# Optimization experiments

Hardware: AMD Instinct MI355X
Metric: run time of the kernel (lower is better)

The kernel has to match this reference:

```python
import jax, jax.numpy as jnp
import numpy as np

B, S, D, H = 2, 2048, 1024, 16
DK = D // H


def setup_inputs() -> dict:
    key = jax.random.key(0)
    ks = jax.random.split(key, 10)
    scale = 1.0 / np.sqrt(D)
    x = jax.random.normal(ks[0], (B, S, D), dtype=jnp.float32)
    # causal mask: 1 = attend, 0 = masked (module's create_causal_mask)
    mask = jnp.tril(jnp.ones((S, S), dtype=jnp.int32))[None, None]
    Wq = jax.random.normal(ks[1], (D, D), jnp.float32) * scale
    bq = jax.random.normal(ks[2], (D,), jnp.float32) * 0.01
    Wk = jax.random.normal(ks[3], (D, D), jnp.float32) * scale
    bk = jax.random.normal(ks[4], (D,), jnp.float32) * 0.01
    Wv = jax.random.normal(ks[5], (D, D), jnp.float32) * scale
    bv = jax.random.normal(ks[6], (D,), jnp.float32) * 0.01
    Wo = jax.random.normal(ks[7], (D, D), jnp.float32) * scale
    bo = jax.random.normal(ks[8], (D,), jnp.float32) * 0.01
    return {"x": x, "mask": mask, "Wq": Wq, "bq": bq, "Wk": Wk, "bk": bk,
            "Wv": Wv, "bv": bv, "Wo": Wo, "bo": bo}


def reference(x, mask, Wq, bq, Wk, bk, Wv, bv, Wo, bo):
    b, s, _ = x.shape
    # projections; [B,S,D] -> [B,H,S,DK]
    def split_heads(t):
        return t.reshape(b, s, H, DK).transpose(0, 2, 1, 3)
    Q = split_heads(x @ Wq + bq)
    K = split_heads(x @ Wk + bk)
    V = split_heads(x @ Wv + bv)
    scores = jnp.einsum('bhqd,bhkd->bhqk', Q, K) / np.sqrt(DK)
    scores = jnp.where(mask == 0, jnp.float32(-1e9), scores)
    attn = jax.nn.softmax(scores, axis=-1)  # dropout p=0 -> identity
    ctx = jnp.einsum('bhqk,bhkd->bhqd', attn, V)
    ctx = ctx.transpose(0, 2, 1, 3).reshape(b, s, D)
    return ctx @ Wo + bo
```

## Files before the change

kernel.cpp:

```cpp
#include <hip/hip_runtime.h>
#include <hip/hip_bf16.h>


typedef _Float16 f16x8 __attribute__((ext_vector_type(8)));
typedef _Float16 f16x4 __attribute__((ext_vector_type(4)));
typedef _Float16 f16x2 __attribute__((ext_vector_type(2)));
typedef float f32x4 __attribute__((ext_vector_type(4)));

#define QSCALE 0.180336880111112f

__device__ __forceinline__ void async_copy16(const _Float16* gsrc,
                                             _Float16* ldst) {
  __builtin_amdgcn_global_load_lds(
      (const __attribute__((address_space(1))) void*)gsrc,
      (__attribute__((address_space(3))) void*)ldst, 16, 0, 0);
}

__global__ __launch_bounds__(256) void prep(
    const float* __restrict__ x, _Float16* __restrict__ xh,
    const float* __restrict__ W0, const float* __restrict__ W1,
    const float* __restrict__ W2, const float* __restrict__ W3,
    _Float16* __restrict__ T0, _Float16* __restrict__ T1,
    _Float16* __restrict__ T2, _Float16* __restrict__ T3) {
  if (blockIdx.x < 4096) {
    int i = (blockIdx.x * 256 + threadIdx.x) * 4;
    float4 v = *(const float4*)(x + i);
    f16x4 o;
    o.x = (_Float16)v.x; o.y = (_Float16)v.y;
    o.z = (_Float16)v.z; o.w = (_Float16)v.w;
    *(f16x4*)(xh + i) = o;
    return;
  }
  const int id = blockIdx.x - 4096;
  const int w = id >> 10, rem = id & 1023;
  const int bx = rem & 31, by = rem >> 5;
  const float* W; _Float16* T;
  switch (w) {
    case 0: W = W0; T = T0; break;
    case 1: W = W1; T = T1; break;
    case 2: W = W2; T = T2; break;
    default: W = W3; T = T3; break;
  }
  __shared__ _Float16 tile[32][33];
  const int tx = threadIdx.x & 31, ty = threadIdx.x >> 5;
  const int n0 = bx * 32, k0 = by * 32;
  for (int i = 0; i < 4; i++) {
    int kk = k0 + ty + i * 8;
    tile[ty + i * 8][tx] = (_Float16)W[(size_t)kk * 1024 + n0 + tx];
  }
  __syncthreads();
  for (int i = 0; i < 4; i++) {
    int nn = n0 + ty + i * 8;
    T[(size_t)nn * 1024 + k0 + tx] = tile[tx][ty + i * 8];
  }
}

__global__ __launch_bounds__(256) void gemm_qkv(
    const _Float16* __restrict__ A, const _Float16* __restrict__ BtAll,
    const float* __restrict__ bq, const float* __restrict__ bk,
    const float* __restrict__ bv, _Float16* __restrict__ Qh,
    _Float16* __restrict__ Kh, _Float16* __restrict__ VT) {
  __shared__ _Float16 As[128 * 32];
  __shared__ _Float16 Bs[128 * 32];
  const int tid = threadIdx.x;
  const int wave = tid >> 6, lane = tid & 63;
  const int lr = lane & 15, lq = lane >> 4;
  const int m0 = blockIdx.x * 128, n0 = blockIdx.y * 128;
  const int rw = (wave & 1) * 64, cw = (wave >> 1) * 64;

  const int sel = blockIdx.y >> 3;
  const float* bias = sel == 0 ? bq : (sel == 1 ? bk : bv);
  const int c0 = n0 & 1023;

  f32x4 acc[4][4] = {};
  const int r0 = wave * 32 + (lane >> 2);
  const int woff = (lane & 3) * 8;

  for (int kt = 0; kt < 1024; kt += 32) {
    __syncthreads();
    async_copy16(A + (size_t)(m0 + r0) * 1024 + kt + woff, As + r0 * 32 + woff);
    async_copy16(A + (size_t)(m0 + r0 + 16) * 1024 + kt + woff,
                 As + (r0 + 16) * 32 + woff);
    async_copy16(BtAll + (size_t)(n0 + r0) * 1024 + kt + woff,
                 Bs + r0 * 32 + woff);
    async_copy16(BtAll + (size_t)(n0 + r0 + 16) * 1024 + kt + woff,
                 Bs + (r0 + 16) * 32 + woff);
    __syncthreads();
    f16x8 af[4], bf[4];
    for (int i = 0; i < 4; i++)
      af[i] = *(const f16x8*)(As + (rw + i * 16 + lr) * 32 + lq * 8);
    for (int j = 0; j < 4; j++)
      bf[j] = *(const f16x8*)(Bs + (cw + j * 16 + lr) * 32 + lq * 8);
    for (int i = 0; i < 4; i++)
      for (int j = 0; j < 4; j++)
        acc[i][j] = __builtin_amdgcn_mfma_f32_16x16x32_f16(af[i], bf[j],
                                                           acc[i][j], 0, 0, 0);
  }

  if (sel == 2) {
    for (int i = 0; i < 4; i++) {
      const int row = m0 + rw + i * 16 + lq * 4;
      const int bb = row >> 11, ss = row & 2047;
      for (int j = 0; j < 4; j++) {
        const int col = c0 + cw + j * 16 + lr;
        const int hh = col >> 6, dk = col & 63;
        const float bvl = bias[col];
        f16x4 pv;
        for (int r = 0; r < 4; r++) pv[r] = (_Float16)(acc[i][j][r] + bvl);
        *(f16x4*)(VT + ((size_t)(bb * 16 + hh) * 64 + dk) * 2048 + ss) = pv;
      }
    }
  } else {
    _Float16* out = sel == 0 ? Qh : Kh;
    const float scl = sel == 0 ? QSCALE : 1.0f;
    for (int i = 0; i < 4; i++) {
      const int row = m0 + rw + i * 16 + lq * 4;
      for (int j = 0; j < 4; j++) {
        const int col = c0 + cw + j * 16 + lr;
        const float bvl = bias[col];
        for (int r = 0; r < 4; r++)
          out[(size_t)(row + r) * 1024 + col] =
              (_Float16)((acc[i][j][r] + bvl) * scl);
      }
    }
  }
}

__global__ __launch_bounds__(256) void gemm_out(
    const _Float16* __restrict__ A, const _Float16* __restrict__ Bt,
    const float* __restrict__ bias, float* __restrict__ out) {
  __shared__ _Float16 As[128 * 32];
  __shared__ _Float16 Bs[64 * 32];
  const int tid = threadIdx.x;
  const int wave = tid >> 6, lane = tid & 63;
  const int lr = lane & 15, lq = lane >> 4;
  const int m0 = blockIdx.x * 128, n0 = blockIdx.y * 64;
  const int rw = (wave & 1) * 64, cw = (wave >> 1) * 32;
  f32x4 acc[4][2] = {};
  const int r0 = wave * 32 + (lane >> 2);
  const int br = tid >> 2;
  const int woff = (lane & 3) * 8;

  for (int kt = 0; kt < 1024; kt += 32) {
    __syncthreads();
    async_copy16(A + (size_t)(m0 + r0) * 1024 + kt + woff, As + r0 * 32 + woff);
    async_copy16(A + (size_t)(m0 + r0 + 16) * 1024 + kt + woff,
                 As + (r0 + 16) * 32 + woff);
    async_copy16(Bt + (size_t)(n0 + br) * 1024 + kt + woff,
                 Bs + br * 32 + woff);
    __syncthreads();
    f16x8 af[4], bf[2];
    for (int i = 0; i < 4; i++)
      af[i] = *(const f16x8*)(As + (rw + i * 16 + lr) * 32 + lq * 8);
    for (int j = 0; j < 2; j++)
      bf[j] = *(const f16x8*)(Bs + (cw + j * 16 + lr) * 32 + lq * 8);
    for (int i = 0; i < 4; i++)
      for (int j = 0; j < 2; j++)
        acc[i][j] = __builtin_amdgcn_mfma_f32_16x16x32_f16(af[i], bf[j],
                                                           acc[i][j], 0, 0, 0);
  }
  for (int i = 0; i < 4; i++) {
    const int row = m0 + rw + i * 16 + lq * 4;
    for (int j = 0; j < 2; j++) {
      const int col = n0 + cw + j * 16 + lr;
      const float bvl = bias[col];
      for (int r = 0; r < 4; r++)
        out[(size_t)(row + r) * 1024 + col] = acc[i][j][r] + bvl;
    }
  }
}

__global__ __launch_bounds__(256) void attn(const _Float16* __restrict__ Q,
                                            const _Float16* __restrict__ K,
                                            const _Float16* __restrict__ VT,
                                            _Float16* __restrict__ ctx) {
  const int qt = 31 - blockIdx.y;
  const int bh = blockIdx.x;
  const int b = bh >> 4, h = bh & 15;
  const int tid = threadIdx.x, wave = tid >> 6, lane = tid & 63;
  const int lr = lane & 15, lq = lane >> 4;
  const int qmin = qt * 64 + wave * 16;
  const size_t qkbase = ((size_t)b * 2048) * 1024 + h * 64;
  const size_t vtbase = ((size_t)bh) * 64 * 2048;

  __shared__ _Float16 Ks[2][64 * 72];
  __shared__ _Float16 Vs[2][64 * 72];

  const _Float16* qp = Q + qkbase + (size_t)(qmin + lr) * 1024 + lq * 8;
  f16x8 qf0 = *(const f16x8*)qp;
  f16x8 qf1 = *(const f16x8*)(qp + 32);

  float mrow = -1e30f, lsum = 0.f;
  f32x4 o[4] = {};

  const int sgr = tid >> 2, sgc = (tid & 3) * 8;
  const _Float16* Kg0 = K + qkbase + (size_t)sgr * 1024 + sgc;
  const _Float16* Vg0 = VT + vtbase + (size_t)sgr * 2048 + sgc;
  uint4 ka = *(const uint4*)Kg0, kb = *(const uint4*)(Kg0 + 32);
  uint4 va = *(const uint4*)Vg0, vb = *(const uint4*)(Vg0 + 32);

  for (int t = 0; t <= qt; t++) {
    _Float16* ksb = Ks[t & 1];
    _Float16* vsb = Vs[t & 1];
    *(uint4*)(ksb + sgr * 72 + sgc) = ka;
    *(uint4*)(ksb + sgr * 72 + sgc + 32) = kb;
    *(uint4*)(vsb + sgr * 72 + sgc) = va;
    *(uint4*)(vsb + sgr * 72 + sgc + 32) = vb;
    __syncthreads();
    if (t < qt) {
      const _Float16* kg = Kg0 + (size_t)(t + 1) * 64 * 1024;
      const _Float16* vg = Vg0 + (t + 1) * 64;
      ka = *(const uint4*)kg; kb = *(const uint4*)(kg + 32);
      va = *(const uint4*)vg; vb = *(const uint4*)(vg + 32);
    }

    const int kv0 = t * 64;
    f32x4 s[4];
    for (int ks = 0; ks < 4; ks++) {
      f16x8 k0 = *(const f16x8*)(ksb + (ks * 16 + lr) * 72 + lq * 8);
      f16x8 k1 = *(const f16x8*)(ksb + (ks * 16 + lr) * 72 + 32 + lq * 8);
      f32x4 z = {};
      z = __builtin_amdgcn_mfma_f32_16x16x32_f16(k0, qf0, z, 0, 0, 0);
      z = __builtin_amdgcn_mfma_f32_16x16x32_f16(k1, qf1, z, 0, 0, 0);
      s[ks] = z;
    }
    if (t == qt) {
      const int qcol = qmin + lr;
      for (int ks = 0; ks < 4; ks++)
        for (int r = 0; r < 4; r++)
          if (kv0 + ks * 16 + lq * 4 + r > qcol) s[ks][r] = -1e30f;
    }
    float mx = s[0][0];
    for (int ks = 0; ks < 4; ks++)
      for (int r = 0; r < 4; r++) mx = fmaxf(mx, s[ks][r]);
    mx = fmaxf(mx, __shfl_xor(mx, 16));
    mx = fmaxf(mx, __shfl_xor(mx, 32));
    float mnew = fmaxf(mrow, mx);
    float alpha = exp2f(mrow - mnew);
    mrow = mnew;
    float rs = 0.f;
    f16x4 pa[4];
    for (int ks = 0; ks < 4; ks++) {
      float p0 = exp2f(s[ks][0] - mnew);
      float p1 = exp2f(s[ks][1] - mnew);
      float p2 = exp2f(s[ks][2] - mnew);
      float p3 = exp2f(s[ks][3] - mnew);
      rs += (p0 + p1) + (p2 + p3);
      f16x2 q01 = __builtin_bit_cast(f16x2, __builtin_amdgcn_cvt_pkrtz(p0, p1));
      f16x2 q23 = __builtin_bit_cast(f16x2, __builtin_amdgcn_cvt_pkrtz(p2, p3));
      pa[ks] = __builtin_shufflevector(q01, q23, 0, 1, 2, 3);
    }
    rs += __shfl_xor(rs, 16);
    rs += __shfl_xor(rs, 32);
    lsum = lsum * alpha + rs;
    if (__any(alpha != 1.0f)) {
      float ar[4];
      for (int r = 0; r < 4; r++) ar[r] = __shfl(alpha, lq * 4 + r);
      for (int dn = 0; dn < 4; dn++)
        for (int r = 0; r < 4; r++) o[dn][r] *= ar[r];
    }
    for (int ks = 0; ks < 4; ks++)
      for (int dn = 0; dn < 4; dn++) {
        f16x4 vf =
            *(const f16x4*)(vsb + (dn * 16 + lr) * 72 + ks * 16 + lq * 4);
        o[dn] =
            __builtin_amdgcn_mfma_f32_16x16x16f16(pa[ks], vf, o[dn], 0, 0, 0);
      }
  }

  for (int r = 0; r < 4; r++) {
    float lv = __shfl(lsum, lq * 4 + r);
    float inv = 1.0f / lv;
    const int row = qmin + lq * 4 + r;
    for (int dn = 0; dn < 4; dn++)
      ctx[qkbase + (size_t)row * 1024 + dn * 16 + lr] =
          (_Float16)(o[dn][r] * inv);
  }
}

extern "C" void kernel_launch(void* const* d_in, const int* in_sizes, int n_in,
                              void* d_out, int out_size, void* d_ws,
                              size_t ws_size, hipStream_t stream) {
  const float* x  = (const float*)d_in[0];
  const float* Wq = (const float*)d_in[2];
  const float* bq = (const float*)d_in[3];
  const float* Wk = (const float*)d_in[4];
  const float* bk = (const float*)d_in[5];
  const float* Wv = (const float*)d_in[6];
  const float* bv = (const float*)d_in[7];
  const float* Wo = (const float*)d_in[8];
  const float* bo = (const float*)d_in[9];
  float* out = (float*)d_out;

  char* ws = (char*)d_ws;
  const size_t MB = 1 << 20;
  _Float16* xh  = (_Float16*)(ws);
  _Float16* WTs = (_Float16*)(ws + 8 * MB);
  _Float16* WqT = WTs;
  _Float16* WkT = (_Float16*)(ws + 10 * MB);
  _Float16* WvT = (_Float16*)(ws + 12 * MB);
  _Float16* WoT = (_Float16*)(ws + 14 * MB);
  _Float16* Qh  = (_Float16*)(ws + 16 * MB);
  _Float16* Kh  = (_Float16*)(ws + 24 * MB);
  _Float16* VT  = (_Float16*)(ws + 32 * MB);
  _Float16* ctx = (_Float16*)(ws);

  prep<<<8192, 256, 0, stream>>>(x, xh, Wq, Wk, Wv, Wo, WqT, WkT, WvT, WoT);
  gemm_qkv<<<dim3(32, 24), 256, 0, stream>>>(xh, WTs, bq, bk, bv, Qh, Kh, VT);
  attn<<<dim3(32, 32), 256, 0, stream>>>(Qh, Kh, VT, ctx);
  gemm_out<<<dim3(32, 16), 256, 0, stream>>>(ctx, WoT, bo, out);
}
```

Measured before the change: 200.3 us.

## Process 128 query rows per attention block to reuse K/V tiles

The attention kernel now gives each wave two 16-row query fragments, so a block covers 128 queries instead of 64 and the grid's query dimension is halved. Every K/V tile loaded into shared memory feeds twice as many MFMAs, which cuts global K/V traffic and barrier count per query. The causal mask now applies whenever the tile crosses the wave's rows rather than only on the last tile. The cost is higher register pressure, only 512 blocks, and more load imbalance across the causal triangle.

```diff
diff --git a/kernel.cpp b/kernel.cpp
--- a/kernel.cpp
+++ b/kernel.cpp
@@ -174,24 +174,28 @@
                                             const _Float16* __restrict__ K,
                                             const _Float16* __restrict__ VT,
                                             _Float16* __restrict__ ctx) {
-  const int qt = 31 - blockIdx.y;
+  const int qt = 15 - blockIdx.y;
   const int bh = blockIdx.x;
   const int b = bh >> 4, h = bh & 15;
   const int tid = threadIdx.x, wave = tid >> 6, lane = tid & 63;
   const int lr = lane & 15, lq = lane >> 4;
-  const int qmin = qt * 64 + wave * 16;
+  const int qmin = qt * 128 + wave * 32;
   const size_t qkbase = ((size_t)b * 2048) * 1024 + h * 64;
   const size_t vtbase = ((size_t)bh) * 64 * 2048;
 
   __shared__ _Float16 Ks[2][64 * 72];
   __shared__ _Float16 Vs[2][64 * 72];
 
-  const _Float16* qp = Q + qkbase + (size_t)(qmin + lr) * 1024 + lq * 8;
-  f16x8 qf0 = *(const f16x8*)qp;
-  f16x8 qf1 = *(const f16x8*)(qp + 32);
-
-  float mrow = -1e30f, lsum = 0.f;
-  f32x4 o[4] = {};
+  f16x8 qf[2][2];
+  for (int m = 0; m < 2; m++) {
+    const _Float16* qp =
+        Q + qkbase + (size_t)(qmin + m * 16 + lr) * 1024 + lq * 8;
+    qf[m][0] = *(const f16x8*)qp;
+    qf[m][1] = *(const f16x8*)(qp + 32);
+  }
+
+  float mrow[2] = {-1e30f, -1e30f}, lsum[2] = {0.f, 0.f};
+  f32x4 o[2][4] = {};
 
   const int sgr = tid >> 2, sgc = (tid & 3) * 8;
   const _Float16* Kg0 = K + qkbase + (size_t)sgr * 1024 + sgc;
@@ -199,7 +203,8 @@
   uint4 ka = *(const uint4*)Kg0, kb = *(const uint4*)(Kg0 + 32);
   uint4 va = *(const uint4*)Vg0, vb = *(const uint4*)(Vg0 + 32);
 
-  for (int t = 0; t <= qt; t++) {
+  const int tmax = 2 * qt + 1;
+  for (int t = 0;; t++) {
     _Float16* ksb = Ks[t & 1];
     _Float16* vsb = Vs[t & 1];
     *(uint4*)(ksb + sgr * 72 + sgc) = ka;
@@ -207,7 +212,7 @@
     *(uint4*)(vsb + sgr * 72 + sgc) = va;
     *(uint4*)(vsb + sgr * 72 + sgc + 32) = vb;
     __syncthreads();
-    if (t < qt) {
+    if (t < tmax) {
       const _Float16* kg = Kg0 + (size_t)(t + 1) * 64 * 1024;
       const _Float16* vg = Vg0 + (t + 1) * 64;
       ka = *(const uint4*)kg; kb = *(const uint4*)(kg + 32);
@@ -215,66 +220,81 @@
     }
 
     const int kv0 = t * 64;
-    f32x4 s[4];
+    f32x4 s[2][4];
     for (int ks = 0; ks < 4; ks++) {
       f16x8 k0 = *(const f16x8*)(ksb + (ks * 16 + lr) * 72 + lq * 8);
       f16x8 k1 = *(const f16x8*)(ksb + (ks * 16 + lr) * 72 + 32 + lq * 8);
-      f32x4 z = {};
-      z = __builtin_amdgcn_mfma_f32_16x16x32_f16(k0, qf0, z, 0, 0, 0);
-      z = __builtin_amdgcn_mfma_f32_16x16x32_f16(k1, qf1, z, 0, 0, 0);
-      s[ks] = z;
-    }
-    if (t == qt) {
-      const int qcol = qmin + lr;
+      for (int m = 0; m < 2; m++) {
+        f32x4 z = {};
+        z = __builtin_amdgcn_mfma_f32_16x16x32_f16(k0, qf[m][0], z, 0, 0, 0);
+        z = __builtin_amdgcn_mfma_f32_16x16x32_f16(k1, qf[m][1], z, 0, 0, 0);
+        s[m][ks] = z;
+      }
+    }
+    if (kv0 + 63 > qmin) {
+      for (int m = 0; m < 2; m++) {
+        const int qcol = qmin + m * 16 + lr;
+        for (int ks = 0; ks < 4; ks++)
+          for (int r = 0; r < 4; r++)
+            if (kv0 + ks * 16 + lq * 4 + r > qcol) s[m][ks][r] = -1e30f;
+      }
+    }
+    f16x4 pa[2][4];
+    float alpha[2];
+    for (int m = 0; m < 2; m++) {
+      float mx = s[m][0][0];
       for (int ks = 0; ks < 4; ks++)
-        for (int r = 0; r < 4; r++)
-          if (kv0 + ks * 16 + lq * 4 + r > qcol) s[ks][r] = -1e30f;
-    }
-    float mx = s[0][0];
-    for (int ks = 0; ks < 4; ks++)
-      for (int r = 0; r < 4; r++) mx = fmaxf(mx, s[ks][r]);
-    mx = fmaxf(mx, __shfl_xor(mx, 16));
-    mx = fmaxf(mx, __shfl_xor(mx, 32));
-    float mnew = fmaxf(mrow, mx);
-    float alpha = exp2f(mrow - mnew);
-    mrow = mnew;
-    float rs = 0.f;
-    f16x4 pa[4];
-    for (int ks = 0; ks < 4; ks++) {
-      float p0 = exp2f(s[ks][0] - mnew);
-      float p1 = exp2f(s[ks][1] - mnew);
-      float p2 = exp2f(s[ks][2] - mnew);
-      float p3 = exp2f(s[ks][3] - mnew);
-      rs += (p0 + p1) + (p2 + p3);
-      f16x2 q01 = __builtin_bit_cast(f16x2, __builtin_amdgcn_cvt_pkrtz(p0, p1));
-      f16x2 q23 = __builtin_bit_cast(f16x2, __builtin_amdgcn_cvt_pkrtz(p2, p3));
-      pa[ks] = __builtin_shufflevector(q01, q23, 0, 1, 2, 3);
-    }
-    rs += __shfl_xor(rs, 16);
-    rs += __shfl_xor(rs, 32);
-    lsum = lsum * alpha + rs;
-    if (__any(alpha != 1.0f)) {
-      float ar[4];
-      for (int r = 0; r < 4; r++) ar[r] = __shfl(alpha, lq * 4 + r);
-      for (int dn = 0; dn < 4; dn++)
-        for (int r = 0; r < 4; r++) o[dn][r] *= ar[r];
+        for (int r = 0; r < 4; r++) mx = fmaxf(mx, s[m][ks][r]);
+      mx = fmaxf(mx, __shfl_xor(mx, 16));
+      mx = fmaxf(mx, __shfl_xor(mx, 32));
+      float mnew = fmaxf(mrow[m], mx);
+      alpha[m] = exp2f(mrow[m] - mnew);
+      mrow[m] = mnew;
+      float rs = 0.f;
+      for (int ks = 0; ks < 4; ks++) {
+        float p0 = exp2f(s[m][ks][0] - mnew);
+        float p1 = exp2f(s[m][ks][1] - mnew);
+        float p2 = exp2f(s[m][ks][2] - mnew);
+        float p3 = exp2f(s[m][ks][3] - mnew);
+        rs += (p0 + p1) + (p2 + p3);
+        f16x2 q01 =
+            __builtin_bit_cast(f16x2, __builtin_amdgcn_cvt_pkrtz(p0, p1));
+        f16x2 q23 =
+            __builtin_bit_cast(f16x2, __builtin_amdgcn_cvt_pkrtz(p2, p3));
+        pa[m][ks] = __builtin_shufflevector(q01, q23, 0, 1, 2, 3);
+      }
+      rs += __shfl_xor(rs, 16);
+      rs += __shfl_xor(rs, 32);
+      lsum[m] = lsum[m] * alpha[m] + rs;
+    }
+    if (__any((alpha[0] != 1.0f) | (alpha[1] != 1.0f))) {
+      for (int m = 0; m < 2; m++) {
+        float ar[4];
+        for (int r = 0; r < 4; r++) ar[r] = __shfl(alpha[m], lq * 4 + r);
+        for (int dn = 0; dn < 4; dn++)
+          for (int r = 0; r < 4; r++) o[m][dn][r] *= ar[r];
+      }
     }
     for (int ks = 0; ks < 4; ks++)
       for (int dn = 0; dn < 4; dn++) {
         f16x4 vf =
             *(const f16x4*)(vsb + (dn * 16 + lr) * 72 + ks * 16 + lq * 4);
-        o[dn] =
-            __builtin_amdgcn_mfma_f32_16x16x16f16(pa[ks], vf, o[dn], 0, 0, 0);
-      }
-  }
-
-  for (int r = 0; r < 4; r++) {
-    float lv = __shfl(lsum, lq * 4 + r);
-    float inv = 1.0f / lv;
-    const int row = qmin + lq * 4 + r;
-    for (int dn = 0; dn < 4; dn++)
-      ctx[qkbase + (size_t)row * 1024 + dn * 16 + lr] =
-          (_Float16)(o[dn][r] * inv);
+        for (int m = 0; m < 2; m++)
+          o[m][dn] = __builtin_amdgcn_mfma_f32_16x16x16f16(pa[m][ks], vf,
+                                                           o[m][dn], 0, 0, 0);
+      }
+    if (t == tmax) break;
+  }
+
+  for (int m = 0; m < 2; m++) {
+    for (int r = 0; r < 4; r++) {
+      float lv = __shfl(lsum[m], lq * 4 + r);
+      float inv = 1.0f / lv;
+      const int row = qmin + m * 16 + lq * 4 + r;
+      for (int dn = 0; dn < 4; dn++)
+        ctx[qkbase + (size_t)row * 1024 + dn * 16 + lr] =
+            (_Float16)(o[m][dn][r] * inv);
+    }
   }
 }
 
@@ -307,6 +327,6 @@
 
   prep<<<8192, 256, 0, stream>>>(x, xh, Wq, Wk, Wv, Wo, WqT, WkT, WvT, WoT);
   gemm_qkv<<<dim3(32, 24), 256, 0, stream>>>(xh, WTs, bq, bk, bv, Qh, Kh, VT);
-  attn<<<dim3(32, 32), 256, 0, stream>>>(Qh, Kh, VT, ctx);
+  attn<<<dim3(32, 16), 256, 0, stream>>>(Qh, Kh, VT, ctx);
   gemm_out<<<dim3(32, 16), 256, 0, stream>>>(ctx, WoT, bo, out);
 }
```

Result: slower. 215.4 us (+7.5%).
